# Kernel optimization log

Hardware: AMD Instinct MI355X
Metric: run time of the kernel (lower is better)

The kernel has to match this reference:

```python
import jax, jax.numpy as jnp
import numpy as np

B, NPG, DEG = 16, 2048, 16          # graphs, nodes per graph, avg degree
N_TOT = B * NPG
E_TOT = N_TOT * DEG
NEG_SLOPE = 0.2


def _gat(x, src, dst, n, w, a_src, a_dst, b):
    # PyG GATConv: concat heads, add self loops, leaky_relu(0.2), segment softmax over targets
    H, C = a_src.shape
    h = (x @ w.T).reshape(n, H, C)                       # [n,H,C]
    sl = jnp.arange(n, dtype=src.dtype)
    s = jnp.concatenate([src, sl])
    d = jnp.concatenate([dst, sl])
    e = jax.nn.leaky_relu((h * a_src).sum(-1)[s] + (h * a_dst).sum(-1)[d], NEG_SLOPE)  # [E+n,H]
    emax = jax.lax.stop_gradient(jax.ops.segment_max(e, d, num_segments=n))
    ee = jnp.exp(e - emax[d])
    alpha = ee / (jax.ops.segment_sum(ee, d, num_segments=n)[d] + 1e-16)
    out = jax.ops.segment_sum(alpha[:, :, None] * h[s], d, num_segments=n)  # [n,H,C]
    return out.reshape(n, H * C) + b


def _gcn(x, src, dst, mask, n, w, b):
    # PyG GCNConv with self loops + symmetric norm; mask = float edge validity
    h = x @ w.T
    deg = jax.ops.segment_sum(mask, dst, num_segments=n) + 1.0  # +1 for self loop
    dinv = jax.lax.rsqrt(deg)
    coef = dinv[src] * dinv[dst] * mask
    out = jax.ops.segment_sum(coef[:, None] * h[src], dst, num_segments=n) + (dinv * dinv)[:, None] * h
    return out + b


def _sag(x, src, dst, mask, b_graphs, npg, k, w_rel, b_rel, w_root):
    # PyG SAGPooling(ratio=0.5): GraphConv score, per-graph top-k, x[perm]*tanh(score[perm]), filter_adj
    n = b_graphs * npg
    agg = jax.ops.segment_sum(mask[:, None] * x[src], dst, num_segments=n)
    score = (agg @ w_rel.T + b_rel + x @ w_root.T)[:, 0]      # [n]
    _, idx = jax.lax.top_k(score.reshape(b_graphs, npg), k)    # [B,k]
    perm = (jnp.arange(b_graphs, dtype=jnp.int32)[:, None] * npg + idx).reshape(-1)
    x_new = x[perm] * jnp.tanh(score[perm])[:, None]
    new_id = jnp.full((n,), -1, jnp.int32).at[perm].set(jnp.arange(b_graphs * k, dtype=jnp.int32))
    ns, nd = new_id[src], new_id[dst]
    valid = mask * ((ns >= 0) & (nd >= 0)).astype(x.dtype)
    return x_new, jnp.maximum(ns, 0), jnp.maximum(nd, 0), valid


def setup_inputs() -> dict:
    key = jax.random.key(0)
    ks = jax.random.split(key, 32)

    def lin(k, o, i):
        return (jax.random.normal(k, (o, i), jnp.float32) / np.sqrt(i)).astype(jnp.float32)

    x = jax.random.normal(ks[0], (N_TOT, 64), jnp.float32)
    off = jnp.repeat(jnp.arange(B, dtype=jnp.int32) * NPG, NPG * DEG)
    src = off + jax.random.randint(ks[1], (E_TOT,), 0, NPG, jnp.int32)
    dst = off + jax.random.randint(ks[2], (E_TOT,), 0, NPG, jnp.int32)
    edge_index = jnp.stack([src, dst])
    batch = jnp.repeat(jnp.arange(B, dtype=jnp.int32), NPG)

    return {
        'x': x, 'edge_index': edge_index, 'batch': batch,
        'gat1_w': lin(ks[3], 256, 64), 'gat1_asrc': lin(ks[4], 4, 64), 'gat1_adst': lin(ks[5], 4, 64),
        'gat1_b': jnp.zeros((256,), jnp.float32),
        'gat2_w': lin(ks[6], 256, 256), 'gat2_asrc': lin(ks[7], 4, 64), 'gat2_adst': lin(ks[8], 4, 64),
        'gat2_b': jnp.zeros((256,), jnp.float32),
        # pooling GCN1: 256 -> 128
        'gcn1_w': lin(ks[9], 128, 256), 'gcn1_b': jnp.zeros((128,), jnp.float32),
        'sag1_wrel': lin(ks[10], 1, 128), 'sag1_brel': jnp.zeros((1,), jnp.float32), 'sag1_wroot': lin(ks[11], 1, 128),
        # pooling GCN2: 128 -> 128
        'gcn2_w': lin(ks[12], 128, 128), 'gcn2_b': jnp.zeros((128,), jnp.float32),
        'sag2_wrel': lin(ks[13], 1, 128), 'sag2_brel': jnp.zeros((1,), jnp.float32), 'sag2_wroot': lin(ks[14], 1, 128),
        # classifier 128 -> 256 -> 128 -> 10
        'fc1_w': lin(ks[15], 256, 128), 'fc1_b': jnp.zeros((256,), jnp.float32),
        'fc2_w': lin(ks[16], 128, 256), 'fc2_b': jnp.zeros((128,), jnp.float32),
        'out_w': lin(ks[17], 10, 128), 'out_b': jnp.zeros((10,), jnp.float32),
    }


def reference(x, edge_index, batch,
              gat1_w, gat1_asrc, gat1_adst, gat1_b,
              gat2_w, gat2_asrc, gat2_adst, gat2_b,
              gcn1_w, gcn1_b, sag1_wrel, sag1_brel, sag1_wroot,
              gcn2_w, gcn2_b, sag2_wrel, sag2_brel, sag2_wroot,
              fc1_w, fc1_b, fc2_w, fc2_b, out_w, out_b):
    n = x.shape[0]
    src, dst = edge_index[0], edge_index[1]
    ones = jnp.ones(src.shape[0], x.dtype)

    # GAT encoder
    h = jax.nn.relu(_gat(x, src, dst, n, gat1_w, gat1_asrc, gat1_adst, gat1_b))
    h = _gat(h, src, dst, n, gat2_w, gat2_asrc, gat2_adst, gat2_b)  # [n,256]

    # GCN + SAGPool x2
    h = jax.nn.relu(_gcn(h, src, dst, ones, n, gcn1_w, gcn1_b))
    k1 = NPG // 2
    h, s1, d1, m1 = _sag(h, src, dst, ones, B, NPG, k1, sag1_wrel, sag1_brel, sag1_wroot)
    h = jax.nn.relu(_gcn(h, s1, d1, m1, B * k1, gcn2_w, gcn2_b))
    k2 = k1 // 2
    h, s2, d2, m2 = _sag(h, s1, d1, m1, B, k1, k2, sag2_wrel, sag2_brel, sag2_wroot)

    # global mean pool (equal-size graphs -> simple reshape-mean; batch vec implied)
    g = h.reshape(B, k2, -1).mean(axis=1)  # [B,128]

    # classifier MLP
    g = jax.nn.relu(g @ fc1_w.T + fc1_b)
    g = jax.nn.relu(g @ fc2_w.T + fc2_b)
    return g @ out_w.T + out_b  # [B,10]
```

## Files before the change

kernel.cpp:

```cpp
#include <hip/hip_runtime.h>

#define N1 32768
#define EE 524288
#define NB 16
#define DEG 16
#define NPG1 2048
#define KK1 1024
#define N2 16384
#define NPG2 1024
#define KK2 512
#define N3 8192

typedef _Float16 half8_t __attribute__((ext_vector_type(8)));
typedef float floatx16 __attribute__((ext_vector_type(16)));

static __device__ __forceinline__ float leaky(float x){ return fmaxf(x, 0.2f*x); }

__global__ void count_split(const int* __restrict__ dst, int* __restrict__ cnt,
                            const float* __restrict__ w0, int n0,
                            const float* __restrict__ w1, int n1,
                            const float* __restrict__ w2, int n2,
                            const float* __restrict__ w3, int n3,
                            _Float16* __restrict__ wh, _Float16* __restrict__ wl){
    int b = blockIdx.x;
    int tid = threadIdx.x;
    if (b < EE/256){
        atomicAdd(&cnt[dst[b*256 + tid]], 1);
    } else {
        int i = (b - EE/256)*256 + tid;
        int n01 = n0 + n1, n012 = n01 + n2, nt = n012 + n3;
        if (i >= nt) return;
        float v = (i < n0) ? w0[i] : (i < n01) ? w1[i - n0] : (i < n012) ? w2[i - n01] : w3[i - n012];
        _Float16 h = (_Float16)v;
        wh[i] = h; wl[i] = (_Float16)(v - (float)h);
    }
}

__global__ void blocksum_k(const int* __restrict__ cnt, int* __restrict__ bs){
    __shared__ int red[4];
    int tid = threadIdx.x;
    int v = cnt[blockIdx.x*256 + tid];
    #pragma unroll
    for (int off = 32; off; off >>= 1) v += __shfl_xor(v, off);
    if ((tid & 63) == 0) red[tid >> 6] = v;
    __syncthreads();
    if (tid == 0) bs[blockIdx.x] = red[0] + red[1] + red[2] + red[3];
}

__global__ void scan_write_k(const int* __restrict__ cnt, const int* __restrict__ bs,
                             int nb, int2* __restrict__ rpx, int* __restrict__ cur,
                             float* __restrict__ dinv){
    __shared__ int sbs[128];
    __shared__ int wsum[4];
    int tid = threadIdx.x;
    int b = blockIdx.x;
    if (tid < nb) sbs[tid] = bs[tid];
    __syncthreads();
    for (int off = 1; off < nb; off <<= 1){
        int v = 0;
        if (tid < nb && tid >= off) v = sbs[tid - off];
        __syncthreads();
        if (tid < nb) sbs[tid] += v;
        __syncthreads();
    }
    int base = (b == 0) ? 0 : sbs[b-1];
    int i = b*256 + tid;
    int c = cnt[i];
    int lane = tid & 63, wv = tid >> 6;
    int x = c;
    #pragma unroll
    for (int off = 1; off < 64; off <<= 1){ int y = __shfl_up(x, off); if (lane >= off) x += y; }
    if (lane == 63) wsum[wv] = x;
    __syncthreads();
    if (tid == 0){ int run = 0; for (int w2 = 0; w2 < 4; w2++){ int t = wsum[w2]; wsum[w2] = run; run += t; } }
    __syncthreads();
    int excl = x - c + wsum[wv];
    int beg = base + excl;
    rpx[i]  = make_int2(beg, beg + c);
    cur[i]  = beg;
    dinv[i] = rsqrtf((float)c + 1.0f);
}

__global__ void scatter1(const int* __restrict__ src, const int* __restrict__ dst,
                         int* __restrict__ cur, int* __restrict__ esrc, int E){
    int i = blockIdx.x*blockDim.x + threadIdx.x;
    if (i < E){ int p = atomicAdd(&cur[dst[i]], 1); esrc[p] = src[i]; }
}

__global__ void csr2_build(const int* __restrict__ perm, const int* __restrict__ nid,
                           const int2* __restrict__ rpx, const int* __restrict__ EL,
                           int2* __restrict__ rpx2, float* __restrict__ dinv2,
                           int* __restrict__ EL2){
    int lane = threadIdx.x & 63;
    int w = threadIdx.x >> 6;
    int d2 = blockIdx.x*4 + w;
    int old = __builtin_amdgcn_readfirstlane(perm[d2]);
    int2 re = rpx[old];
    int beg = re.x, end = re.y;
    unsigned long long below = (1ull << lane) - 1ull;
    int cnt = 0;
    for (int i = beg; i < end; i += 64){
        int ii = i + lane;
        int sn = -1;
        if (ii < end) sn = nid[EL[ii]];
        bool take = sn >= 0;
        unsigned long long m = __ballot(take);
        int pos = cnt + __popcll(m & below);
        if (take) EL2[beg + pos] = sn;
        cnt += __popcll(m);
    }
    if (lane == 0){
        rpx2[d2] = make_int2(beg, beg + cnt);
        dinv2[d2] = rsqrtf((float)cnt + 1.0f);
    }
}

#define KS 64
static __device__ __forceinline__ int ldsoff(int row, int k8){
    return row*64 + ((k8 ^ (row & 7)) << 3);
}

__global__ __launch_bounds__(256, 2) void gemm_h2(const float* __restrict__ A,
        const _Float16* __restrict__ WHp, const _Float16* __restrict__ WLp,
        float* __restrict__ C, int n, int K, int M,
        const int* __restrict__ perm, const float* __restrict__ tt){
    __shared__ _Float16 sm[4*128*KS];
    _Float16* sAH = sm;
    _Float16* sAL = sm + 128*KS;
    _Float16* sWH = sm + 2*128*KS;
    _Float16* sWL = sm + 3*128*KS;
    int t = threadIdx.x;
    int lane = t & 63;
    int wid = t >> 6;
    int wr = wid >> 1, wc = wid & 1;
    int row0 = blockIdx.x*128, col0 = blockIdx.y*128;
    int srow = t >> 3;
    int sk8  = t & 7;

    floatx16 acc[2][2];
    #pragma unroll
    for (int i = 0; i < 2; i++)
        #pragma unroll
        for (int j = 0; j < 2; j++)
            #pragma unroll
            for (int q = 0; q < 16; q++) acc[i][j][q] = 0.f;

    for (int kk = 0; kk < K; kk += KS){
        #pragma unroll
        for (int p = 0; p < 4; p++){
            int r = srow + p*32;
            int rr = row0 + r;
            int arow = perm ? perm[rr] : rr;
            float tscale = perm ? tt[rr] : 1.0f;
            const float* ga = A + (size_t)arow*K + kk + sk8*8;
            float4 a0 = *(const float4*)ga;
            float4 a1 = *(const float4*)(ga + 4);
            half8_t ahi, alo;
            float av[8] = {a0.x,a0.y,a0.z,a0.w,a1.x,a1.y,a1.z,a1.w};
            #pragma unroll
            for (int q = 0; q < 8; q++){
                float v = av[q] * tscale;
                _Float16 h = (_Float16)v;
                ahi[q] = h; alo[q] = (_Float16)(v - (float)h);
            }
            size_t wo = (size_t)(col0 + r)*K + kk + sk8*8;
            half8_t whi = *(const half8_t*)(WHp + wo);
            half8_t wlo = *(const half8_t*)(WLp + wo);
            int o = ldsoff(r, sk8);
            *(half8_t*)&sAH[o] = ahi;
            *(half8_t*)&sAL[o] = alo;
            *(half8_t*)&sWH[o] = whi;
            *(half8_t*)&sWL[o] = wlo;
        }
        __syncthreads();
        #pragma unroll
        for (int kc = 0; kc < 4; kc++){
            int k8 = kc*2 + (lane >> 5);
            int ra = wr*64 + (lane & 31);
            int rb = wc*64 + (lane & 31);
            half8_t ah0 = *(const half8_t*)&sAH[ldsoff(ra,      k8)];
            half8_t ah1 = *(const half8_t*)&sAH[ldsoff(ra + 32, k8)];
            half8_t al0 = *(const half8_t*)&sAL[ldsoff(ra,      k8)];
            half8_t al1 = *(const half8_t*)&sAL[ldsoff(ra + 32, k8)];
            half8_t bh0 = *(const half8_t*)&sWH[ldsoff(rb,      k8)];
            half8_t bh1 = *(const half8_t*)&sWH[ldsoff(rb + 32, k8)];
            half8_t bl0 = *(const half8_t*)&sWL[ldsoff(rb,      k8)];
            half8_t bl1 = *(const half8_t*)&sWL[ldsoff(rb + 32, k8)];
            acc[0][0] = __builtin_amdgcn_mfma_f32_32x32x16_f16(ah0, bh0, acc[0][0], 0,0,0);
            acc[0][0] = __builtin_amdgcn_mfma_f32_32x32x16_f16(ah0, bl0, acc[0][0], 0,0,0);
            acc[0][0] = __builtin_amdgcn_mfma_f32_32x32x16_f16(al0, bh0, acc[0][0], 0,0,0);
            acc[0][1] = __builtin_amdgcn_mfma_f32_32x32x16_f16(ah0, bh1, acc[0][1], 0,0,0);
            acc[0][1] = __builtin_amdgcn_mfma_f32_32x32x16_f16(ah0, bl1, acc[0][1], 0,0,0);
            acc[0][1] = __builtin_amdgcn_mfma_f32_32x32x16_f16(al0, bh1, acc[0][1], 0,0,0);
            acc[1][0] = __builtin_amdgcn_mfma_f32_32x32x16_f16(ah1, bh0, acc[1][0], 0,0,0);
            acc[1][0] = __builtin_amdgcn_mfma_f32_32x32x16_f16(ah1, bl0, acc[1][0], 0,0,0);
            acc[1][0] = __builtin_amdgcn_mfma_f32_32x32x16_f16(al1, bh0, acc[1][0], 0,0,0);
            acc[1][1] = __builtin_amdgcn_mfma_f32_32x32x16_f16(ah1, bh1, acc[1][1], 0,0,0);
            acc[1][1] = __builtin_amdgcn_mfma_f32_32x32x16_f16(ah1, bl1, acc[1][1], 0,0,0);
            acc[1][1] = __builtin_amdgcn_mfma_f32_32x32x16_f16(al1, bh1, acc[1][1], 0,0,0);
        }
        __syncthreads();
    }
    #pragma unroll
    for (int rt = 0; rt < 2; rt++)
        #pragma unroll
        for (int ct = 0; ct < 2; ct++){
            int baser = row0 + wr*64 + rt*32 + 4*(lane >> 5);
            int c = col0 + wc*64 + ct*32 + (lane & 31);
            #pragma unroll
            for (int r = 0; r < 16; r++){
                int rr = baser + (r & 3) + 8*(r >> 2);
                C[(size_t)rr*M + c] = acc[rt][ct][r];
            }
        }
}

__global__ void attn_pre(const float* __restrict__ h, const float* __restrict__ wsrc,
                         const float* __restrict__ wdst, float* __restrict__ as_,
                         float* __restrict__ ad_){
    int lane = threadIdx.x & 63;
    int w = threadIdx.x >> 6;
    int d = blockIdx.x*4 + w;
    float4 hv = *(const float4*)(h + (size_t)d*256 + lane*4);
    float4 ws = *(const float4*)(wsrc + lane*4);
    float4 wd = *(const float4*)(wdst + lane*4);
    float ps = hv.x*ws.x + hv.y*ws.y + hv.z*ws.z + hv.w*ws.w;
    float pd = hv.x*wd.x + hv.y*wd.y + hv.z*wd.z + hv.w*wd.w;
    #pragma unroll
    for (int m = 8; m; m >>= 1){ ps += __shfl_xor(ps, m); pd += __shfl_xor(pd, m); }
    if ((lane & 15) == 0){
        as_[d*4 + (lane >> 4)] = ps;
        ad_[d*4 + (lane >> 4)] = pd;
    }
}

template<int RELU>
__global__ void gat_agg(const float* __restrict__ h, const float* __restrict__ as_,
                        const float* __restrict__ ad_, const float* __restrict__ bias,
                        const int2* __restrict__ rpx, const int* __restrict__ esrc,
                        float* __restrict__ out){
    int lane = threadIdx.x & 63;
    int nb = gridDim.x;
    int b = blockIdx.x;
    int sb = (b & 7)*(nb >> 3) + (b >> 3);
    int d = __builtin_amdgcn_readfirstlane(sb*4 + (int)(threadIdx.x >> 6));
    int2 re = rpx[d];
    int beg = re.x, end = re.y;

    int hh = lane >> 4;
    float adh = ad_[(d<<2) + hh];
    float aself = as_[(d<<2) + hh];

    float dn[4];
    dn[0] = __expf(leaky(aself + adh)); dn[1] = 0.f; dn[2] = 0.f; dn[3] = 0.f;
    float4 hd = ((const float4*)(h + ((size_t)d<<8)))[lane];
    float4 AX[4];
    AX[0].x = dn[0]*hd.x; AX[0].y = dn[0]*hd.y; AX[0].z = dn[0]*hd.z; AX[0].w = dn[0]*hd.w;
    AX[1] = {0,0,0,0}; AX[2] = {0,0,0,0}; AX[3] = {0,0,0,0};

    int i = beg;
    int endu = beg + ((end - beg) & ~7);
    for (; i < endu; i += 8){
        int s_[8];
        #pragma unroll
        for (int j = 0; j < 8; j++) s_[j] = __builtin_amdgcn_readfirstlane(esrc[i + j]);
        float a_[8];
        #pragma unroll
        for (int j = 0; j < 8; j++) a_[j] = as_[(s_[j]<<2) + hh];
        float4 hv_[8];
        #pragma unroll
        for (int j = 0; j < 8; j++) hv_[j] = ((const float4*)(h + ((size_t)s_[j]<<8)))[lane];
        #pragma unroll
        for (int j = 0; j < 8; j++){
            float x = a_[j] + adh;
            float p = __expf(fmaxf(x, 0.2f*x));
            dn[j & 3] += p;
            AX[j & 3].x = fmaf(p, hv_[j].x, AX[j & 3].x);
            AX[j & 3].y = fmaf(p, hv_[j].y, AX[j & 3].y);
            AX[j & 3].z = fmaf(p, hv_[j].z, AX[j & 3].z);
            AX[j & 3].w = fmaf(p, hv_[j].w, AX[j & 3].w);
        }
    }
    for (; i < end; ++i){
        int s = __builtin_amdgcn_readfirstlane(esrc[i]);
        float x = as_[(s<<2) + hh] + adh;
        float4 hv = ((const float4*)(h + ((size_t)s<<8)))[lane];
        float p = __expf(fmaxf(x, 0.2f*x));
        dn[0] += p;
        AX[0].x = fmaf(p, hv.x, AX[0].x); AX[0].y = fmaf(p, hv.y, AX[0].y);
        AX[0].z = fmaf(p, hv.z, AX[0].z); AX[0].w = fmaf(p, hv.w, AX[0].w);
    }
    float den = ((dn[0] + dn[1]) + (dn[2] + dn[3])) + 1e-16f;
    float r = 1.0f / den;
    int c0 = lane*4;
    float4 bv = *(const float4*)(bias + c0);
    float4 acc;
    acc.x = ((AX[0].x+AX[1].x)+(AX[2].x+AX[3].x))*r + bv.x;
    acc.y = ((AX[0].y+AX[1].y)+(AX[2].y+AX[3].y))*r + bv.y;
    acc.z = ((AX[0].z+AX[1].z)+(AX[2].z+AX[3].z))*r + bv.z;
    acc.w = ((AX[0].w+AX[1].w)+(AX[2].w+AX[3].w))*r + bv.w;
    if (RELU){
        acc.x = fmaxf(acc.x, 0.f); acc.y = fmaxf(acc.y, 0.f);
        acc.z = fmaxf(acc.z, 0.f); acc.w = fmaxf(acc.w, 0.f);
    }
    ((float4*)(out + ((size_t)d<<8)))[lane] = acc;
}

__global__ void gcn_agg_sag(const float* __restrict__ h, const float* __restrict__ dinv,
                            const float* __restrict__ bias,
                            const float* __restrict__ wrel, const float* __restrict__ wroot,
                            const float* __restrict__ brel,
                            const int2* __restrict__ rpx, const int* __restrict__ esrc,
                            float* __restrict__ out, float* __restrict__ Y, float* __restrict__ Z){
    int lane = threadIdx.x & 63;
    int nb = gridDim.x;
    int b = blockIdx.x;
    int sb = (b & 7)*(nb >> 3) + (b >> 3);
    int d = __builtin_amdgcn_readfirstlane(sb*4 + (int)(threadIdx.x >> 6));
    int2 re = rpx[d];
    int beg = re.x, end = re.y;
    float dv = dinv[d];
    int c0 = lane*2;
    float2 hd = ((const float2*)(h + ((size_t)d<<7)))[lane];
    float self = dv*dv;
    float ax[4] = {self*hd.x, 0.f, 0.f, 0.f};
    float ay[4] = {self*hd.y, 0.f, 0.f, 0.f};
    int i = beg;
    int endu = beg + ((end - beg) & ~7);
    for (; i < endu; i += 8){
        int s_[8];
        #pragma unroll
        for (int j = 0; j < 8; j++) s_[j] = __builtin_amdgcn_readfirstlane(esrc[i + j]);
        float di_[8];
        #pragma unroll
        for (int j = 0; j < 8; j++) di_[j] = dinv[s_[j]];
        float2 hv_[8];
        #pragma unroll
        for (int j = 0; j < 8; j++) hv_[j] = ((const float2*)(h + ((size_t)s_[j]<<7)))[lane];
        #pragma unroll
        for (int j = 0; j < 8; j++){
            float coef = di_[j]*dv;
            ax[j & 3] = fmaf(coef, hv_[j].x, ax[j & 3]);
            ay[j & 3] = fmaf(coef, hv_[j].y, ay[j & 3]);
        }
    }
    for (; i < end; ++i){
        int s = __builtin_amdgcn_readfirstlane(esrc[i]);
        float coef = dinv[s]*dv;
        float2 hv = ((const float2*)(h + ((size_t)s<<7)))[lane];
        ax[0] = fmaf(coef, hv.x, ax[0]); ay[0] = fmaf(coef, hv.y, ay[0]);
    }
    float axs = ((ax[0]+ax[1])+(ax[2]+ax[3]));
    float ays = ((ay[0]+ay[1])+(ay[2]+ay[3]));
    axs = fmaxf(axs + bias[c0], 0.f);
    ays = fmaxf(ays + bias[c0+1], 0.f);
    float2 o; o.x = axs; o.y = ays;
    ((float2*)(out + ((size_t)d<<7)))[lane] = o;
    float py = axs*wrel[c0]  + ays*wrel[c0+1];
    float pz = axs*wroot[c0] + ays*wroot[c0+1];
    #pragma unroll
    for (int off = 32; off; off >>= 1){ py += __shfl_xor(py, off); pz += __shfl_xor(pz, off); }
    if (lane == 0){ Y[d] = py; Z[d] = pz + brel[0]; }
}

__global__ void sag_lite(const float* __restrict__ Y, const float* __restrict__ Z,
                         const int2* __restrict__ rpx, const int* __restrict__ esrc,
                         float* __restrict__ score){
    int lane = threadIdx.x & 63;
    int w = threadIdx.x >> 6;
    int nb = gridDim.x;
    int b = blockIdx.x;
    int sb = (b & 7)*(nb >> 3) + (b >> 3);
    int d = sb*4 + w;
    int2 re = rpx[d];
    float s = 0.f;
    for (int i = re.x + lane; i < re.y; i += 64) s += Y[esrc[i]];
    #pragma unroll
    for (int off = 32; off; off >>= 1) s += __shfl_xor(s, off);
    if (lane == 0) score[d] = s + Z[d];
}

__global__ __launch_bounds__(64) void topk_wave(const float* __restrict__ score,
        int npg, int k, int* __restrict__ perm, float* __restrict__ ssort,
        int* __restrict__ nid, int writeNid){
    __shared__ unsigned keys[2048];
    __shared__ int hist[256];
    int g = blockIdx.x;
    int lane = threadIdx.x;
    int nch = npg >> 6;
    for (int c = 0; c < nch; c++){
        unsigned u = __float_as_uint(score[g*npg + c*64 + lane]);
        keys[c*64 + lane] = (u & 0x80000000u) ? ~u : (u | 0x80000000u);
    }
    int need = k;
    unsigned prefix = 0u, pmask = 0u;
    #pragma unroll
    for (int shift = 24; shift >= 0; shift -= 8){
        #pragma unroll
        for (int q = 0; q < 4; q++) hist[lane*4 + q] = 0;
        for (int c = 0; c < nch; c++){
            unsigned u = keys[c*64 + lane];
            if ((u & pmask) == prefix) atomicAdd(&hist[(u >> shift) & 255u], 1);
        }
        int h0 = hist[lane*4], h1 = hist[lane*4+1], h2 = hist[lane*4+2], h3 = hist[lane*4+3];
        int s3 = h3, s2 = h2 + s3, s1 = h1 + s2, s0 = h0 + s1;
        int tot = s0;
        int suf = tot;
        #pragma unroll
        for (int off = 1; off < 64; off <<= 1){
            int v = __shfl_down(suf, off);
            if (lane + off < 64) suf += v;
        }
        int above_quad = suf - tot;
        int c0 = s0 + above_quad, c1 = s1 + above_quad, c2 = s2 + above_quad, c3 = s3 + above_quad;
        int sel = -1;
        if (c0 >= need && c1 < need) sel = 0;
        if (c1 >= need && c2 < need) sel = 1;
        if (c2 >= need && c3 < need) sel = 2;
        if (c3 >= need && above_quad < need) sel = 3;
        unsigned long long msk = __ballot(sel >= 0);
        int srcl = __ffsll((long long)msk) - 1;
        int binq = __shfl(sel, srcl);
        int bin = srcl*4 + binq;
        int cge_next = (binq == 0) ? __shfl(c1, srcl) :
                       (binq == 1) ? __shfl(c2, srcl) :
                       (binq == 2) ? __shfl(c3, srcl) : __shfl(above_quad, srcl);
        need -= cge_next;
        prefix |= ((unsigned)bin) << shift;
        pmask  |= 255u << shift;
    }
    unsigned thr = prefix;
    int m = need;
    unsigned long long below = (lane == 63) ? 0x7FFFFFFFFFFFFFFFull : ((1ull << lane) - 1ull);
    int base = 0, eqbase = 0;
    for (int c = 0; c < nch; c++){
        unsigned u = keys[c*64 + lane];
        bool gt = u > thr;
        bool eq = (u == thr);
        unsigned long long meq = __ballot(eq);
        int eqrank = eqbase + __popcll(meq & below);
        bool take = gt || (eq && eqrank < m);
        unsigned long long mtk = __ballot(take);
        int pos = base + __popcll(mtk & below);
        int node = g*npg + c*64 + lane;
        if (take){
            perm[g*k + pos] = node;
            ssort[g*k + pos] = tanhf(score[node]);
            if (writeNid) nid[node] = g*k + pos;
        } else if (writeNid) nid[node] = -1;
        base += __popcll(mtk);
        eqbase += __popcll(meq);
    }
}

__global__ void pool_mlp(const float* __restrict__ x, const int* __restrict__ perm,
                         const float* __restrict__ ssort,
                         const float* __restrict__ fc1w, const float* __restrict__ fc1b,
                         const float* __restrict__ fc2w, const float* __restrict__ fc2b,
                         const float* __restrict__ ow,  const float* __restrict__ ob,
                         float* __restrict__ out){
    __shared__ float tt[KK2];
    __shared__ float part[128];
    __shared__ float gv[128], t1[256], t2[128];
    int b = blockIdx.x, t = threadIdx.x;
    tt[t]       = ssort[b*KK2 + t];
    tt[t + 256] = ssort[b*KK2 + t + 256];
    __syncthreads();
    int c = t & 127, half = t >> 7;
    float s = 0.f;
    #pragma unroll 4
    for (int i = half*256; i < half*256 + 256; i++){
        int o = perm[b*KK2 + i];
        s = fmaf(tt[i], x[(size_t)o*128 + c], s);
    }
    if (half) part[c] = s;
    __syncthreads();
    if (!half) gv[c] = (s + part[c]) * (1.0f/KK2);
    __syncthreads();
    {
        float s1 = fc1b[t];
        for (int cc = 0; cc < 128; cc++) s1 += gv[cc]*fc1w[t*128 + cc];
        t1[t] = fmaxf(s1, 0.f);
    }
    __syncthreads();
    if (t < 128){
        float s2 = fc2b[t];
        for (int cc = 0; cc < 256; cc++) s2 += t1[cc]*fc2w[t*256 + cc];
        t2[t] = fmaxf(s2, 0.f);
    }
    __syncthreads();
    if (t < 10){
        float s3 = ob[t];
        for (int cc = 0; cc < 128; cc++) s3 += t2[cc]*ow[t*128 + cc];
        out[b*10 + t] = s3;
    }
}

extern "C" void kernel_launch(void* const* d_in, const int* in_sizes, int n_in,
                              void* d_out, int out_size, void* d_ws, size_t ws_size,
                              hipStream_t stream){
    (void)in_sizes; (void)n_in; (void)out_size; (void)ws_size;
    const float* x    = (const float*)d_in[0];
    const int*   eidx = (const int*)d_in[1];
    const int*   src  = eidx;
    const int*   dst  = eidx + EE;
    const float* g1w  = (const float*)d_in[3];
    const float* g1as = (const float*)d_in[4];
    const float* g1ad = (const float*)d_in[5];
    const float* g1b  = (const float*)d_in[6];
    const float* g2w  = (const float*)d_in[7];
    const float* g2as = (const float*)d_in[8];
    const float* g2ad = (const float*)d_in[9];
    const float* g2b  = (const float*)d_in[10];
    const float* c1w  = (const float*)d_in[11];
    const float* c1b  = (const float*)d_in[12];
    const float* s1wrel  = (const float*)d_in[13];
    const float* s1brel  = (const float*)d_in[14];
    const float* s1wroot = (const float*)d_in[15];
    const float* c2w  = (const float*)d_in[16];
    const float* c2b  = (const float*)d_in[17];
    const float* s2wrel  = (const float*)d_in[18];
    const float* s2brel  = (const float*)d_in[19];
    const float* s2wroot = (const float*)d_in[20];
    const float* f1w  = (const float*)d_in[21];
    const float* f1b  = (const float*)d_in[22];
    const float* f2w  = (const float*)d_in[23];
    const float* f2b  = (const float*)d_in[24];
    const float* ow   = (const float*)d_in[25];
    const float* ob   = (const float*)d_in[26];
    float* out = (float*)d_out;

    char* ws = (char*)d_ws;
    size_t off = 0;
    auto alloc = [&](size_t bytes)->char*{
        char* p = ws + off;
        off += (bytes + 255) & ~(size_t)255;
        return p;
    };
    float* F0     = (float*)alloc((size_t)N1*256*4);
    float* F1     = (float*)alloc((size_t)N1*256*4);
    float* F2     = (float*)alloc((size_t)N2*128*4);
    float* AS     = (float*)alloc((size_t)N1*4*4);
    float* AD     = (float*)alloc((size_t)N1*4*4);
    int2*  RPX    = (int2*) alloc((size_t)N1*8);
    int*   CUR    = (int*)  alloc((size_t)N1*4);
    int*   EL     = (int*)  alloc((size_t)EE*4);
    float* DINV   = (float*)alloc((size_t)N1*4);
    float* SCORE  = (float*)alloc((size_t)N1*4);
    float* Y      = (float*)alloc((size_t)N1*4);
    float* Z      = (float*)alloc((size_t)N1*4);
    int*   PERM1  = (int*)  alloc((size_t)N2*4);
    float* SSORT1 = (float*)alloc((size_t)N2*4);
    int*   NID    = (int*)  alloc((size_t)N1*4);
    int2*  RPX2   = (int2*) alloc((size_t)N2*8);
    int*   EL2    = (int*)  alloc((size_t)EE*4);
    float* DINV2  = (float*)alloc((size_t)N2*4);
    int*   PERM2  = (int*)  alloc((size_t)N3*4);
    float* SSORT2 = (float*)alloc((size_t)N3*4);
    int*   BS     = (int*)  alloc((size_t)128*4);
    _Float16* WH  = (_Float16*)alloc((size_t)131072*2);
    _Float16* WL  = (_Float16*)alloc((size_t)131072*2);
    const int o_g1 = 0, o_g2 = 16384, o_c1 = 81920, o_c2 = 114688;

    hipMemsetAsync(CUR, 0, (size_t)N1*4, stream);
    count_split<<<EE/256 + 512, 256, 0, stream>>>(dst, CUR,
        g1w, 16384, g2w, 65536, c1w, 32768, c2w, 16384, WH, WL);
    blocksum_k<<<N1/256, 256, 0, stream>>>(CUR, BS);
    scan_write_k<<<N1/256, 256, 0, stream>>>(CUR, BS, N1/256, RPX, CUR, DINV);
    scatter1<<<EE/256, 256, 0, stream>>>(src, dst, CUR, EL, EE);

    gemm_h2<<<dim3(N1/128, 2), 256, 0, stream>>>(x, WH + o_g1, WL + o_g1, F0, N1, 64, 256, nullptr, nullptr);
    attn_pre<<<N1/4, 256, 0, stream>>>(F0, g1as, g1ad, AS, AD);
    gat_agg<1><<<N1/4, 256, 0, stream>>>(F0, AS, AD, g1b, RPX, EL, F1);

    gemm_h2<<<dim3(N1/128, 2), 256, 0, stream>>>(F1, WH + o_g2, WL + o_g2, F0, N1, 256, 256, nullptr, nullptr);
    attn_pre<<<N1/4, 256, 0, stream>>>(F0, g2as, g2ad, AS, AD);
    gat_agg<0><<<N1/4, 256, 0, stream>>>(F0, AS, AD, g2b, RPX, EL, F1);

    gemm_h2<<<dim3(N1/128, 1), 256, 0, stream>>>(F1, WH + o_c1, WL + o_c1, F0, N1, 256, 128, nullptr, nullptr);
    gcn_agg_sag<<<N1/4, 256, 0, stream>>>(F0, DINV, c1b, s1wrel, s1wroot, s1brel,
                                          RPX, EL, F1, Y, Z);

    sag_lite<<<N1/4, 256, 0, stream>>>(Y, Z, RPX, EL, SCORE);
    topk_wave<<<NB, 64, 0, stream>>>(SCORE, NPG1, KK1, PERM1, SSORT1, NID, 1);

    csr2_build<<<N2/4, 256, 0, stream>>>(PERM1, NID, RPX, EL, RPX2, DINV2, EL2);

    gemm_h2<<<dim3(N2/128, 1), 256, 0, stream>>>(F1, WH + o_c2, WL + o_c2, F0, N2, 128, 128, PERM1, SSORT1);
    gcn_agg_sag<<<N2/4, 256, 0, stream>>>(F0, DINV2, c2b, s2wrel, s2wroot, s2brel,
                                          RPX2, EL2, F2, Y, Z);

    sag_lite<<<N2/4, 256, 0, stream>>>(Y, Z, RPX2, EL2, SCORE);
    topk_wave<<<NB, 64, 0, stream>>>(SCORE, NPG2, KK2, PERM2, SSORT2, nullptr, 0);

    pool_mlp<<<NB, 256, 0, stream>>>(F2, PERM2, SSORT2,
                                     f1w, f1b, f2w, f2b, ow, ob, out);
}
```

Before: 314.8 us.

## Use fixed-capacity adjacency slots and fuse attention logits into GEMM epilogue

Replaces the count/blocksum/scan/scatter CSR build with one atomic scatter into fixed 64-slot per-node edge lists. Row bounds and GCN degree normalisation now come directly from the counts. Separately, the GAT attention dot-products (attn_pre) move into the GEMM epilogue using cross-lane shuffle reductions, which removes two kernels and a re-read of the features. The cost is that a node with in-degree above 64 would overflow into its neighbour's slots, and the edge-list buffers become larger and sparser.

```diff
diff --git a/kernel.cpp b/kernel.cpp
--- a/kernel.cpp
+++ b/kernel.cpp
@@ -10,22 +10,27 @@
 #define NPG2 1024
 #define KK2 512
 #define N3 8192
+#define CAP 64
 
 typedef _Float16 half8_t __attribute__((ext_vector_type(8)));
 typedef float floatx16 __attribute__((ext_vector_type(16)));
 
 static __device__ __forceinline__ float leaky(float x){ return fmaxf(x, 0.2f*x); }
 
-__global__ void count_split(const int* __restrict__ dst, int* __restrict__ cnt,
-                            const float* __restrict__ w0, int n0,
-                            const float* __restrict__ w1, int n1,
-                            const float* __restrict__ w2, int n2,
-                            const float* __restrict__ w3, int n3,
-                            _Float16* __restrict__ wh, _Float16* __restrict__ wl){
+__global__ void scatter_split(const int* __restrict__ src, const int* __restrict__ dst,
+                              int* __restrict__ cnt, int* __restrict__ esrc,
+                              const float* __restrict__ w0, int n0,
+                              const float* __restrict__ w1, int n1,
+                              const float* __restrict__ w2, int n2,
+                              const float* __restrict__ w3, int n3,
+                              _Float16* __restrict__ wh, _Float16* __restrict__ wl){
     int b = blockIdx.x;
     int tid = threadIdx.x;
     if (b < EE/256){
-        atomicAdd(&cnt[dst[b*256 + tid]], 1);
+        int i = b*256 + tid;
+        int d = dst[i];
+        int p = atomicAdd(&cnt[d], 1);
+        esrc[(d << 6) + p] = src[i];
     } else {
         int i = (b - EE/256)*256 + tid;
         int n01 = n0 + n1, n012 = n01 + n2, nt = n012 + n3;
@@ -36,82 +41,31 @@
     }
 }
 
-__global__ void blocksum_k(const int* __restrict__ cnt, int* __restrict__ bs){
-    __shared__ int red[4];
-    int tid = threadIdx.x;
-    int v = cnt[blockIdx.x*256 + tid];
-    #pragma unroll
-    for (int off = 32; off; off >>= 1) v += __shfl_xor(v, off);
-    if ((tid & 63) == 0) red[tid >> 6] = v;
-    __syncthreads();
-    if (tid == 0) bs[blockIdx.x] = red[0] + red[1] + red[2] + red[3];
-}
-
-__global__ void scan_write_k(const int* __restrict__ cnt, const int* __restrict__ bs,
-                             int nb, int2* __restrict__ rpx, int* __restrict__ cur,
-                             float* __restrict__ dinv){
-    __shared__ int sbs[128];
-    __shared__ int wsum[4];
-    int tid = threadIdx.x;
-    int b = blockIdx.x;
-    if (tid < nb) sbs[tid] = bs[tid];
-    __syncthreads();
-    for (int off = 1; off < nb; off <<= 1){
-        int v = 0;
-        if (tid < nb && tid >= off) v = sbs[tid - off];
-        __syncthreads();
-        if (tid < nb) sbs[tid] += v;
-        __syncthreads();
-    }
-    int base = (b == 0) ? 0 : sbs[b-1];
-    int i = b*256 + tid;
-    int c = cnt[i];
-    int lane = tid & 63, wv = tid >> 6;
-    int x = c;
-    #pragma unroll
-    for (int off = 1; off < 64; off <<= 1){ int y = __shfl_up(x, off); if (lane >= off) x += y; }
-    if (lane == 63) wsum[wv] = x;
-    __syncthreads();
-    if (tid == 0){ int run = 0; for (int w2 = 0; w2 < 4; w2++){ int t = wsum[w2]; wsum[w2] = run; run += t; } }
-    __syncthreads();
-    int excl = x - c + wsum[wv];
-    int beg = base + excl;
-    rpx[i]  = make_int2(beg, beg + c);
-    cur[i]  = beg;
-    dinv[i] = rsqrtf((float)c + 1.0f);
-}
-
-__global__ void scatter1(const int* __restrict__ src, const int* __restrict__ dst,
-                         int* __restrict__ cur, int* __restrict__ esrc, int E){
-    int i = blockIdx.x*blockDim.x + threadIdx.x;
-    if (i < E){ int p = atomicAdd(&cur[dst[i]], 1); esrc[p] = src[i]; }
-}
-
 __global__ void csr2_build(const int* __restrict__ perm, const int* __restrict__ nid,
-                           const int2* __restrict__ rpx, const int* __restrict__ EL,
+                           const int* __restrict__ cnt, const int* __restrict__ EL,
                            int2* __restrict__ rpx2, float* __restrict__ dinv2,
                            int* __restrict__ EL2){
     int lane = threadIdx.x & 63;
     int w = threadIdx.x >> 6;
     int d2 = blockIdx.x*4 + w;
     int old = __builtin_amdgcn_readfirstlane(perm[d2]);
-    int2 re = rpx[old];
-    int beg = re.x, end = re.y;
+    int beg = old << 6;
+    int end = beg + cnt[old];
     unsigned long long below = (1ull << lane) - 1ull;
-    int cnt = 0;
+    int c2 = 0;
     for (int i = beg; i < end; i += 64){
         int ii = i + lane;
         int sn = -1;
         if (ii < end) sn = nid[EL[ii]];
         bool take = sn >= 0;
         unsigned long long m = __ballot(take);
-        int pos = cnt + __popcll(m & below);
+        int pos = c2 + __popcll(m & below);
         if (take) EL2[beg + pos] = sn;
-        cnt += __popcll(m);
+        c2 += __popcll(m);
     }
     if (lane == 0){
-        rpx2[d2] = make_int2(beg, beg + cnt);
-        dinv2[d2] = rsqrtf((float)cnt + 1.0f);
+        rpx2[d2] = make_int2(beg, beg + c2);
+        dinv2[d2] = rsqrtf((float)c2 + 1.0f);
     }
 }
 
@@ -123,7 +77,9 @@
 __global__ __launch_bounds__(256, 2) void gemm_h2(const float* __restrict__ A,
         const _Float16* __restrict__ WHp, const _Float16* __restrict__ WLp,
         float* __restrict__ C, int n, int K, int M,
-        const int* __restrict__ perm, const float* __restrict__ tt){
+        const int* __restrict__ perm, const float* __restrict__ tt,
+        const float* __restrict__ asrc, const float* __restrict__ adst,
+        float* __restrict__ AS, float* __restrict__ AD){
     __shared__ _Float16 sm[4*128*KS];
     _Float16* sAH = sm;
     _Float16* sAL = sm + 128*KS;
@@ -213,39 +169,53 @@
                 C[(size_t)rr*M + c] = acc[rt][ct][r];
             }
         }
-}
-
-__global__ void attn_pre(const float* __restrict__ h, const float* __restrict__ wsrc,
-                         const float* __restrict__ wdst, float* __restrict__ as_,
-                         float* __restrict__ ad_){
-    int lane = threadIdx.x & 63;
-    int w = threadIdx.x >> 6;
-    int d = blockIdx.x*4 + w;
-    float4 hv = *(const float4*)(h + (size_t)d*256 + lane*4);
-    float4 ws = *(const float4*)(wsrc + lane*4);
-    float4 wd = *(const float4*)(wdst + lane*4);
-    float ps = hv.x*ws.x + hv.y*ws.y + hv.z*ws.z + hv.w*ws.w;
-    float pd = hv.x*wd.x + hv.y*wd.y + hv.z*wd.z + hv.w*wd.w;
-    #pragma unroll
-    for (int m = 8; m; m >>= 1){ ps += __shfl_xor(ps, m); pd += __shfl_xor(pd, m); }
-    if ((lane & 15) == 0){
-        as_[d*4 + (lane >> 4)] = ps;
-        ad_[d*4 + (lane >> 4)] = pd;
+    if (asrc){
+        int hh = (col0 >> 6) + wc;
+        float a_s0 = asrc[col0 + wc*64 +  0 + (lane & 31)];
+        float a_s1 = asrc[col0 + wc*64 + 32 + (lane & 31)];
+        float a_d0 = adst[col0 + wc*64 +  0 + (lane & 31)];
+        float a_d1 = adst[col0 + wc*64 + 32 + (lane & 31)];
+        #pragma unroll
+        for (int rt = 0; rt < 2; rt++){
+            floatx16 vs, vd;
+            #pragma unroll
+            for (int r = 0; r < 16; r++){
+                vs[r] = acc[rt][0][r]*a_s0 + acc[rt][1][r]*a_s1;
+                vd[r] = acc[rt][0][r]*a_d0 + acc[rt][1][r]*a_d1;
+            }
+            #pragma unroll
+            for (int off = 1; off < 32; off <<= 1){
+                #pragma unroll
+                for (int r = 0; r < 16; r++){
+                    vs[r] += __shfl_xor(vs[r], off);
+                    vd[r] += __shfl_xor(vd[r], off);
+                }
+            }
+            if ((lane & 31) == 0){
+                int baser = row0 + wr*64 + rt*32 + 4*(lane >> 5);
+                #pragma unroll
+                for (int r = 0; r < 16; r++){
+                    int rr = baser + (r & 3) + 8*(r >> 2);
+                    AS[rr*4 + hh] = vs[r];
+                    AD[rr*4 + hh] = vd[r];
+                }
+            }
+        }
     }
 }
 
 template<int RELU>
 __global__ void gat_agg(const float* __restrict__ h, const float* __restrict__ as_,
                         const float* __restrict__ ad_, const float* __restrict__ bias,
-                        const int2* __restrict__ rpx, const int* __restrict__ esrc,
+                        const int* __restrict__ cnt, const int* __restrict__ esrc,
                         float* __restrict__ out){
     int lane = threadIdx.x & 63;
     int nb = gridDim.x;
     int b = blockIdx.x;
     int sb = (b & 7)*(nb >> 3) + (b >> 3);
     int d = __builtin_amdgcn_readfirstlane(sb*4 + (int)(threadIdx.x >> 6));
-    int2 re = rpx[d];
-    int beg = re.x, end = re.y;
+    int beg = d << 6;
+    int end = beg + cnt[d];
 
     int hh = lane >> 4;
     float adh = ad_[(d<<2) + hh];
@@ -306,20 +276,28 @@
     ((float4*)(out + ((size_t)d<<8)))[lane] = acc;
 }
 
-__global__ void gcn_agg_sag(const float* __restrict__ h, const float* __restrict__ dinv,
+template<int MODE>
+__global__ void gcn_agg_sag(const float* __restrict__ h, const int* __restrict__ cnt,
+                            const int2* __restrict__ rpx, const float* __restrict__ dinv,
                             const float* __restrict__ bias,
                             const float* __restrict__ wrel, const float* __restrict__ wroot,
                             const float* __restrict__ brel,
-                            const int2* __restrict__ rpx, const int* __restrict__ esrc,
+                            const int* __restrict__ esrc,
                             float* __restrict__ out, float* __restrict__ Y, float* __restrict__ Z){
     int lane = threadIdx.x & 63;
     int nb = gridDim.x;
     int b = blockIdx.x;
     int sb = (b & 7)*(nb >> 3) + (b >> 3);
     int d = __builtin_amdgcn_readfirstlane(sb*4 + (int)(threadIdx.x >> 6));
-    int2 re = rpx[d];
-    int beg = re.x, end = re.y;
-    float dv = dinv[d];
+    int beg, end;
+    float dv;
+    if (MODE == 0){
+        beg = d << 6; end = beg + cnt[d];
+        dv = rsqrtf((float)(end - beg) + 1.0f);
+    } else {
+        int2 re = rpx[d]; beg = re.x; end = re.y;
+        dv = dinv[d];
+    }
     int c0 = lane*2;
     float2 hd = ((const float2*)(h + ((size_t)d<<7)))[lane];
     float self = dv*dv;
@@ -333,7 +311,10 @@
         for (int j = 0; j < 8; j++) s_[j] = __builtin_amdgcn_readfirstlane(esrc[i + j]);
         float di_[8];
         #pragma unroll
-        for (int j = 0; j < 8; j++) di_[j] = dinv[s_[j]];
+        for (int j = 0; j < 8; j++){
+            if (MODE == 0) di_[j] = rsqrtf((float)cnt[s_[j]] + 1.0f);
+            else           di_[j] = dinv[s_[j]];
+        }
         float2 hv_[8];
         #pragma unroll
         for (int j = 0; j < 8; j++) hv_[j] = ((const float2*)(h + ((size_t)s_[j]<<7)))[lane];
@@ -346,7 +327,8 @@
     }
     for (; i < end; ++i){
         int s = __builtin_amdgcn_readfirstlane(esrc[i]);
-        float coef = dinv[s]*dv;
+        float di = (MODE == 0) ? rsqrtf((float)cnt[s] + 1.0f) : dinv[s];
+        float coef = di*dv;
         float2 hv = ((const float2*)(h + ((size_t)s<<7)))[lane];
         ax[0] = fmaf(coef, hv.x, ax[0]); ay[0] = fmaf(coef, hv.y, ay[0]);
     }
@@ -363,18 +345,21 @@
     if (lane == 0){ Y[d] = py; Z[d] = pz + brel[0]; }
 }
 
+template<int MODE>
 __global__ void sag_lite(const float* __restrict__ Y, const float* __restrict__ Z,
-                         const int2* __restrict__ rpx, const int* __restrict__ esrc,
-                         float* __restrict__ score){
+                         const int* __restrict__ cnt, const int2* __restrict__ rpx,
+                         const int* __restrict__ esrc, float* __restrict__ score){
     int lane = threadIdx.x & 63;
     int w = threadIdx.x >> 6;
     int nb = gridDim.x;
     int b = blockIdx.x;
     int sb = (b & 7)*(nb >> 3) + (b >> 3);
     int d = sb*4 + w;
-    int2 re = rpx[d];
+    int beg, end;
+    if (MODE == 0){ beg = d << 6; end = beg + cnt[d]; }
+    else { int2 re = rpx[d]; beg = re.x; end = re.y; }
     float s = 0.f;
-    for (int i = re.x + lane; i < re.y; i += 64) s += Y[esrc[i]];
+    for (int i = beg + lane; i < end; i += 64) s += Y[esrc[i]];
     #pragma unroll
     for (int off = 32; off; off >>= 1) s += __shfl_xor(s, off);
     if (lane == 0) score[d] = s + Z[d];
@@ -431,7 +416,7 @@
     }
     unsigned thr = prefix;
     int m = need;
-    unsigned long long below = (lane == 63) ? 0x7FFFFFFFFFFFFFFFull : ((1ull << lane) - 1ull);
+    unsigned long long below = (1ull << lane) - 1ull;
     int base = 0, eqbase = 0;
     for (int c = 0; c < nch; c++){
         unsigned u = keys[c*64 + lane];
@@ -542,10 +527,8 @@
     float* F2     = (float*)alloc((size_t)N2*128*4);
     float* AS     = (float*)alloc((size_t)N1*4*4);
     float* AD     = (float*)alloc((size_t)N1*4*4);
-    int2*  RPX    = (int2*) alloc((size_t)N1*8);
-    int*   CUR    = (int*)  alloc((size_t)N1*4);
-    int*   EL     = (int*)  alloc((size_t)EE*4);
-    float* DINV   = (float*)alloc((size_t)N1*4);
+    int*   CNT    = (int*)  alloc((size_t)N1*4);
+    int*   EL     = (int*)  alloc((size_t)N1*CAP*4);
     float* SCORE  = (float*)alloc((size_t)N1*4);
     float* Y      = (float*)alloc((size_t)N1*4);
     float* Z      = (float*)alloc((size_t)N1*4);
@@ -553,44 +536,42 @@
     float* SSORT1 = (float*)alloc((size_t)N2*4);
     int*   NID    = (int*)  alloc((size_t)N1*4);
     int2*  RPX2   = (int2*) alloc((size_t)N2*8);
-    int*   EL2    = (int*)  alloc((size_t)EE*4);
+    int*   EL2    = (int*)  alloc((size_t)N1*CAP*4);
     float* DINV2  = (float*)alloc((size_t)N2*4);
     int*   PERM2  = (int*)  alloc((size_t)N3*4);
     float* SSORT2 = (float*)alloc((size_t)N3*4);
-    int*   BS     = (int*)  alloc((size_t)128*4);
     _Float16* WH  = (_Float16*)alloc((size_t)131072*2);
     _Float16* WL  = (_Float16*)alloc((size_t)131072*2);
     const int o_g1 = 0, o_g2 = 16384, o_c1 = 81920, o_c2 = 114688;
 
-    hipMemsetAsync(CUR, 0, (size_t)N1*4, stream);
-    count_split<<<EE/256 + 512, 256, 0, stream>>>(dst, CUR,
+    hipMemsetAsync(CNT, 0, (size_t)N1*4, stream);
+    scatter_split<<<EE/256 + 512, 256, 0, stream>>>(src, dst, CNT, EL,
         g1w, 16384, g2w, 65536, c1w, 32768, c2w, 16384, WH, WL);
-    blocksum_k<<<N1/256, 256, 0, stream>>>(CUR, BS);
-    scan_write_k<<<N1/256, 256, 0, stream>>>(CUR, BS, N1/256, RPX, CUR, DINV);
-    scatter1<<<EE/256, 256, 0, stream>>>(src, dst, CUR, EL, EE);
-
-    gemm_h2<<<dim3(N1/128, 2), 256, 0, stream>>>(x, WH + o_g1, WL + o_g1, F0, N1, 64, 256, nullptr, nullptr);
-    attn_pre<<<N1/4, 256, 0, stream>>>(F0, g1as, g1ad, AS, AD);
-    gat_agg<1><<<N1/4, 256, 0, stream>>>(F0, AS, AD, g1b, RPX, EL, F1);
-
-    gemm_h2<<<dim3(N1/128, 2), 256, 0, stream>>>(F1, WH + o_g2, WL + o_g2, F0, N1, 256, 256, nullptr, nullptr);
-    attn_pre<<<N1/4, 256, 0, stream>>>(F0, g2as, g2ad, AS, AD);
-    gat_agg<0><<<N1/4, 256, 0, stream>>>(F0, AS, AD, g2b, RPX, EL, F1);
-
-    gemm_h2<<<dim3(N1/128, 1), 256, 0, stream>>>(F1, WH + o_c1, WL + o_c1, F0, N1, 256, 128, nullptr, nullptr);
-    gcn_agg_sag<<<N1/4, 256, 0, stream>>>(F0, DINV, c1b, s1wrel, s1wroot, s1brel,
-                                          RPX, EL, F1, Y, Z);
-
-    sag_lite<<<N1/4, 256, 0, stream>>>(Y, Z, RPX, EL, SCORE);
+
+    gemm_h2<<<dim3(N1/128, 2), 256, 0, stream>>>(x, WH + o_g1, WL + o_g1, F0, N1, 64, 256,
+                                                 nullptr, nullptr, g1as, g1ad, AS, AD);
+    gat_agg<1><<<N1/4, 256, 0, stream>>>(F0, AS, AD, g1b, CNT, EL, F1);
+
+    gemm_h2<<<dim3(N1/128, 2), 256, 0, stream>>>(F1, WH + o_g2, WL + o_g2, F0, N1, 256, 256,
+                                                 nullptr, nullptr, g2as, g2ad, AS, AD);
+    gat_agg<0><<<N1/4, 256, 0, stream>>>(F0, AS, AD, g2b, CNT, EL, F1);
+
+    gemm_h2<<<dim3(N1/128, 1), 256, 0, stream>>>(F1, WH + o_c1, WL + o_c1, F0, N1, 256, 128,
+                                                 nullptr, nullptr, nullptr, nullptr, nullptr, nullptr);
+    gcn_agg_sag<0><<<N1/4, 256, 0, stream>>>(F0, CNT, nullptr, nullptr, c1b,
+                                             s1wrel, s1wroot, s1brel, EL, F1, Y, Z);
+
+    sag_lite<0><<<N1/4, 256, 0, stream>>>(Y, Z, CNT, nullptr, EL, SCORE);
     topk_wave<<<NB, 64, 0, stream>>>(SCORE, NPG1, KK1, PERM1, SSORT1, NID, 1);
 
-    csr2_build<<<N2/4, 256, 0, stream>>>(PERM1, NID, RPX, EL, RPX2, DINV2, EL2);
-
-    gemm_h2<<<dim3(N2/128, 1), 256, 0, stream>>>(F1, WH + o_c2, WL + o_c2, F0, N2, 128, 128, PERM1, SSORT1);
-    gcn_agg_sag<<<N2/4, 256, 0, stream>>>(F0, DINV2, c2b, s2wrel, s2wroot, s2brel,
-                                          RPX2, EL2, F2, Y, Z);
-
-    sag_lite<<<N2/4, 256, 0, stream>>>(Y, Z, RPX2, EL2, SCORE);
+    csr2_build<<<N2/4, 256, 0, stream>>>(PERM1, NID, CNT, EL, RPX2, DINV2, EL2);
+
+    gemm_h2<<<dim3(N2/128, 1), 256, 0, stream>>>(F1, WH + o_c2, WL + o_c2, F0, N2, 128, 128,
+                                                 PERM1, SSORT1, nullptr, nullptr, nullptr, nullptr);
+    gcn_agg_sag<1><<<N2/4, 256, 0, stream>>>(F0, nullptr, RPX2, DINV2, c2b,
+                                             s2wrel, s2wroot, s2brel, EL2, F2, Y, Z);
+
+    sag_lite<1><<<N2/4, 256, 0, stream>>>(Y, Z, nullptr, RPX2, EL2, SCORE);
     topk_wave<<<NB, 64, 0, stream>>>(SCORE, NPG2, KK2, PERM2, SSORT2, nullptr, 0);
 
     pool_mlp<<<NB, 256, 0, stream>>>(F2, PERM2, SSORT2,
```

Measured after the change: 289.6 us. -8.0%, faster.
